# Kernel tuning notes

Hardware: AMD Instinct MI355X
Metric: run time of the kernel (lower is better)

## Reference

```python
import jax, jax.numpy as jnp
import numpy as np

DIM = 2048
RANK = 128


def _xavier_uniform(key, shape, gain=0.5):
    fan_out, fan_in = shape
    limit = gain * np.sqrt(6.0 / (fan_in + fan_out))
    return jax.random.uniform(key, shape, jnp.float32, -limit, limit)


def setup_inputs() -> dict:
    key = jax.random.key(0)
    ks = jax.random.split(key, 6)
    T, B = 1024, 16
    x = jax.random.normal(ks[0], (T, B, DIM), jnp.float32)
    h0 = jax.random.normal(ks[1], (B, DIM), jnp.float32)
    U_x = _xavier_uniform(ks[2], (DIM, RANK))
    V_x = _xavier_uniform(ks[3], (RANK, DIM))
    U_d = _xavier_uniform(ks[4], (DIM, RANK))
    V_d = _xavier_uniform(ks[5], (RANK, DIM))
    r_h = jnp.full((DIM,), 0.9, jnp.float32)
    r_delta = jnp.full((DIM,), 0.1, jnp.float32)
    b = jnp.zeros((DIM,), jnp.float32)
    b_delta = jnp.full((DIM,), -2.0, jnp.float32)
    b_gate = jnp.zeros((DIM,), jnp.float32)
    return {"x": x, "h0": h0, "U_x": U_x, "V_x": V_x, "U_d": U_d, "V_d": V_d,
            "r_h": r_h, "r_delta": r_delta, "b": b, "b_delta": b_delta, "b_gate": b_gate}


def reference(x, h0, U_x, V_x, U_d, V_d, r_h, r_delta, b, b_delta, b_gate):
    # Precompute input projections for all timesteps (batched low-rank GEMMs):
    # W(x) = U @ (V @ x)  ->  [T,B,D]
    wx = jnp.einsum('tbd,rd,or->tbo', x, V_x, U_x)
    wd = jnp.einsum('tbd,rd,or->tbo', x, V_d, U_d)

    def step(h_prev, inp):
        x_t, wx_t, wd_t = inp
        cand = jnp.tanh(r_h * h_prev + wx_t + b)
        delta = jax.nn.sigmoid(wd_t + r_delta * h_prev + b_delta)
        h_new = (1.0 - delta) * h_prev + delta * cand
        g = h_new + x_t + b_gate
        out = h_new * (g * jax.nn.sigmoid(g))  # silu gate
        return h_new, (out, h_new)

    _, (output, hs) = jax.lax.scan(step, h0, (x, wx, wd))
    h = jnp.concatenate([h0[None], hs], axis=0)  # [T+1,B,D]
    return output, h
```

## Files before the change

kernel.cpp:

```cpp
#include <hip/hip_runtime.h>

#define DIMN 2048
#define RANKN 128
#define TT 1024
#define BBATCH 16
#define BD (BBATCH * DIMN)
#define CH 16
#define PADW 68

typedef __attribute__((ext_vector_type(4))) float floatx4;
typedef __attribute__((ext_vector_type(8))) short short8;

__device__ __forceinline__ short f2bf(float f) {
    unsigned u = __float_as_uint(f);
    unsigned r = (u + 0x7FFFu + ((u >> 16) & 1u)) >> 16;
    return (short)r;
}
__device__ __forceinline__ float fast_sigmoid(float z) {
    return 1.0f / (1.0f + __expf(-z));
}
__device__ __forceinline__ float fast_tanh(float z) {
    return 1.0f - 2.0f / (__expf(2.0f * z) + 1.0f);
}

__global__ __launch_bounds__(256)
void prep_vb(const float* __restrict__ Vx, const float* __restrict__ Vd,
             short* __restrict__ Vb) {
    const int gid = blockIdx.x * 256 + threadIdx.x;
    const size_t base = (size_t)gid * 8;
    const size_t half = (size_t)RANKN * DIMN;
    const float* src = (base < half) ? Vx : Vd;
    const size_t off = (base < half) ? base : (base - half);
    float4 a = *(const float4*)(src + off);
    float4 c = *(const float4*)(src + off + 4);
    short8 v;
    v[0] = f2bf(a.x); v[1] = f2bf(a.y); v[2] = f2bf(a.z); v[3] = f2bf(a.w);
    v[4] = f2bf(c.x); v[5] = f2bf(c.y); v[6] = f2bf(c.z); v[7] = f2bf(c.w);
    *(short8*)(Vb + base) = v;
}

__global__ __launch_bounds__(256, 2)
void gemm_xv(const float* __restrict__ X, const short* __restrict__ Vb,
             short* __restrict__ xvb) {
    constexpr int PADK = 40;
    __shared__ short As[32 * PADK];
    __shared__ short Bs[2][128 * PADK];

    const int m0 = blockIdx.x * 32;
    const int tid = threadIdx.x;
    const int wave = tid >> 6;
    const int lane = tid & 63;
    const int lr = lane & 15;
    const int q  = lane >> 4;
    const int mat = wave >> 1;
    const int wn  = (wave & 1) * 64;

    floatx4 acc[2][4] = {};

    for (int k0 = 0; k0 < DIMN; k0 += 32) {
        {
            int r = tid >> 3, c = (tid & 7) * 4;
            float4 v = *(const float4*)(X + (size_t)(m0 + r) * DIMN + k0 + c);
            *(short4*)&As[r * PADK + c] =
                make_short4(f2bf(v.x), f2bf(v.y), f2bf(v.z), f2bf(v.w));
        }
        #pragma unroll
        for (int i = 0; i < 4; ++i) {
            int u = tid + i * 256;
            int bm = u >> 9;
            int rem = u & 511;
            int r = rem >> 2, c8 = (rem & 3) * 8;
            short8 v = *(const short8*)(Vb + ((size_t)bm * RANKN + r) * DIMN + k0 + c8);
            *(short8*)&Bs[bm][r * PADK + c8] = v;
        }
        __syncthreads();

        short8 af[2], bfr[4];
        #pragma unroll
        for (int mi = 0; mi < 2; ++mi)
            af[mi] = *(const short8*)&As[(mi * 16 + lr) * PADK + q * 8];
        #pragma unroll
        for (int nj = 0; nj < 4; ++nj)
            bfr[nj] = *(const short8*)&Bs[mat][(wn + nj * 16 + lr) * PADK + q * 8];

        #pragma unroll
        for (int mi = 0; mi < 2; ++mi)
            #pragma unroll
            for (int nj = 0; nj < 4; ++nj)
                acc[mi][nj] = __builtin_amdgcn_mfma_f32_16x16x32_bf16(
                    af[mi], bfr[nj], acc[mi][nj], 0, 0, 0);
        __syncthreads();
    }

    #pragma unroll
    for (int mi = 0; mi < 2; ++mi)
        #pragma unroll
        for (int nj = 0; nj < 4; ++nj)
            #pragma unroll
            for (int r = 0; r < 4; ++r) {
                int row = m0 + mi * 16 + q * 4 + r;
                int col = mat * RANKN + wn + nj * 16 + lr;
                xvb[(size_t)row * 256 + col] = f2bf(acc[mi][nj][r]);
            }
}

#define SPIN(ctr, tgt) \
    while (((volatile int*)cnt)[ctr] < (tgt)) __builtin_amdgcn_s_sleep(1); \
    asm volatile("" ::: "memory");

#define SIGNAL(ctr, val) \
    asm volatile("" ::: "memory"); \
    if (lane == 0) ((volatile int*)cnt)[ctr] = (val);

#define SIGNAL_AFTER_READS(ctr, val) \
    asm volatile("s_waitcnt lgkmcnt(0)" ::: "memory"); \
    if (lane == 0) ((volatile int*)cnt)[ctr] = (val);

__global__ __launch_bounds__(192, 2)
void fused_scan(const short* __restrict__ xvb, const float* __restrict__ x,
                const float* __restrict__ h0,
                const float* __restrict__ Ux, const float* __restrict__ Ud,
                const float* __restrict__ r_h, const float* __restrict__ r_delta,
                const float* __restrict__ bvec, const float* __restrict__ b_delta,
                const float* __restrict__ b_gate,
                float* __restrict__ obuf, float* __restrict__ hbuf) {
    __shared__ float wxs[2][CH * PADW];
    __shared__ float wds[2][CH * PADW];
    __shared__ float hsh[2][CH * PADW];
    __shared__ short8 Ulds[2][4][4][64];
    __shared__ int cnt[4];

    const int id   = blockIdx.x;
    const int xcd  = id & 7;
    const int slot = id >> 3;
    const int b  = xcd * 2 + (slot & 1);
    const int d0 = (slot >> 1) * 64;

    const int tid  = threadIdx.x;
    const int wave = tid >> 6;
    const int lane = tid & 63;
    const int lr = lane & 15;
    const int q  = lane >> 4;

    if (tid == 0) { cnt[0] = 0; cnt[1] = 0; cnt[2] = 0; cnt[3] = 0; }
    __syncthreads();

    if (wave == 1) {
        #pragma unroll
        for (int mat = 0; mat < 2; ++mat) {
            const float* Up = mat ? Ud : Ux;
            #pragma unroll
            for (int nj = 0; nj < 4; ++nj) {
                const size_t dd = (size_t)(d0 + nj * 16 + lr);
                #pragma unroll
                for (int ks = 0; ks < 4; ++ks) {
                    const int k = ks * 32 + q * 8;
                    float4 u0 = *(const float4*)&Up[dd * RANKN + k];
                    float4 u1 = *(const float4*)&Up[dd * RANKN + k + 4];
                    short8 v;
                    v[0] = f2bf(u0.x); v[1] = f2bf(u0.y);
                    v[2] = f2bf(u0.z); v[3] = f2bf(u0.w);
                    v[4] = f2bf(u1.x); v[5] = f2bf(u1.y);
                    v[6] = f2bf(u1.z); v[7] = f2bf(u1.w);
                    Ulds[mat][nj][ks][lane] = v;
                }
            }
        }
        short8 afp[2][4];
        {
            const size_t row = (size_t)lr * BBATCH + b;
            #pragma unroll
            for (int mat = 0; mat < 2; ++mat)
                #pragma unroll
                for (int ks = 0; ks < 4; ++ks)
                    afp[mat][ks] = *(const short8*)
                        &xvb[row * 256 + mat * RANKN + ks * 32 + q * 8];
        }
        for (int ch = 0; ch < 64; ++ch) {
            if (ch >= 2) { SPIN(1, ch - 1) }
            const int pb = ch & 1;
            #pragma unroll
            for (int mat = 0; mat < 2; ++mat) {
                float* outp = mat ? wds[pb] : wxs[pb];
                #pragma unroll
                for (int nj = 0; nj < 4; ++nj) {
                    floatx4 acc = {};
                    #pragma unroll
                    for (int ks = 0; ks < 4; ++ks)
                        acc = __builtin_amdgcn_mfma_f32_16x16x32_bf16(
                            afp[mat][ks], Ulds[mat][nj][ks][lane], acc, 0, 0, 0);
                    #pragma unroll
                    for (int r = 0; r < 4; ++r)
                        outp[(q * 4 + r) * PADW + nj * 16 + lr] = acc[r];
                }
            }
            SIGNAL(0, ch + 1)
            if (ch < 63) {
                const size_t row = (size_t)((ch + 1) * CH + lr) * BBATCH + b;
                #pragma unroll
                for (int mat = 0; mat < 2; ++mat)
                    #pragma unroll
                    for (int ks = 0; ks < 4; ++ks)
                        afp[mat][ks] = *(const short8*)
                            &xvb[row * 256 + mat * RANKN + ks * 32 + q * 8];
            }
        }
    } else if (wave == 0) {
        const int d = d0 + lane;
        const size_t xo = (size_t)b * DIMN + d;
        const float rh  = r_h[d];
        const float rd  = r_delta[d];
        const float bb  = bvec[d];
        const float bdl = b_delta[d];
        float h = h0[xo];

        for (int ch = 0; ch < 64; ++ch) {
            SPIN(0, ch + 1)
            const int pb = ch & 1;
            float wxr[CH], wdr[CH];
            #pragma unroll
            for (int s = 0; s < CH; ++s) {
                wxr[s] = wxs[pb][s * PADW + lane];
                wdr[s] = wds[pb][s * PADW + lane];
            }
            SIGNAL_AFTER_READS(1, ch + 1)
            if (ch >= 2) { SPIN(3, ch - 1) }
            #pragma unroll
            for (int s = 0; s < CH; ++s) {
                const float cand  = fast_tanh(rh * h + wxr[s] + bb);
                const float delta = fast_sigmoid(wdr[s] + rd * h + bdl);
                h = (1.0f - delta) * h + delta * cand;
                hsh[pb][s * PADW + lane] = h;
            }
            SIGNAL(2, ch + 1)
        }
    } else {
        const int dq  = lane & 15;
        const int tof = lane >> 4;
        const size_t xoffF = (size_t)b * DIMN + d0 + dq * 4;
        const float4 bg4 = *(const float4*)&b_gate[d0 + dq * 4];
        {
            const int dl = d0 + lane;
            (void)dl;
            float4 hv = *(const float4*)&h0[(size_t)b * DIMN + d0 + dq * 4
                                            + (size_t)tof * 0];
            if (tof == 0)
                *(float4*)&hbuf[(size_t)b * DIMN + d0 + dq * 4] = hv;
        }
        float4 xpre[4];
        #pragma unroll
        for (int jj = 0; jj < 4; ++jj)
            xpre[jj] = *(const float4*)&x[(size_t)(jj * 4 + tof) * BD + xoffF];

        for (int ch = 0; ch < 64; ++ch) {
            SPIN(2, ch + 1)
            const int pb = ch & 1;
            float4 hv[4];
            #pragma unroll
            for (int jj = 0; jj < 4; ++jj)
                hv[jj] = *(const float4*)&hsh[pb][(jj * 4 + tof) * PADW + dq * 4];
            SIGNAL_AFTER_READS(3, ch + 1)
            const int tb = ch * CH;
            #pragma unroll
            for (int jj = 0; jj < 4; ++jj) {
                const int t = jj * 4 + tof;
                const float4 xv = xpre[jj];
                float4 ov;
                float g0 = hv[jj].x + xv.x + bg4.x;
                ov.x = hv[jj].x * (g0 * fast_sigmoid(g0));
                float g1 = hv[jj].y + xv.y + bg4.y;
                ov.y = hv[jj].y * (g1 * fast_sigmoid(g1));
                float g2 = hv[jj].z + xv.z + bg4.z;
                ov.z = hv[jj].z * (g2 * fast_sigmoid(g2));
                float g3 = hv[jj].w + xv.w + bg4.w;
                ov.w = hv[jj].w * (g3 * fast_sigmoid(g3));
                *(float4*)&obuf[(size_t)(tb + t) * BD + xoffF] = ov;
                *(float4*)&hbuf[(size_t)(tb + t + 1) * BD + xoffF] = hv[jj];
            }
            if (ch < 63) {
                const int tn = (ch + 1) * CH;
                #pragma unroll
                for (int jj = 0; jj < 4; ++jj)
                    xpre[jj] = *(const float4*)
                        &x[(size_t)(tn + jj * 4 + tof) * BD + xoffF];
            }
        }
    }
}

extern "C" void kernel_launch(void* const* d_in, const int* in_sizes, int n_in,
                              void* d_out, int out_size, void* d_ws, size_t ws_size,
                              hipStream_t stream) {
    const float* x       = (const float*)d_in[0];
    const float* h0      = (const float*)d_in[1];
    const float* U_x     = (const float*)d_in[2];
    const float* V_x     = (const float*)d_in[3];
    const float* U_d     = (const float*)d_in[4];
    const float* V_d     = (const float*)d_in[5];
    const float* r_h     = (const float*)d_in[6];
    const float* r_delta = (const float*)d_in[7];
    const float* bvec    = (const float*)d_in[8];
    const float* b_delta = (const float*)d_in[9];
    const float* b_gate  = (const float*)d_in[10];

    float* obuf = (float*)d_out;
    float* hbuf = obuf + (size_t)TT * BD;
    short* xvb  = (short*)d_ws;
    short* Vb   = xvb + (size_t)TT * BBATCH * 256;

    prep_vb<<<256, 256, 0, stream>>>(V_x, V_d, Vb);

    gemm_xv<<<TT * BBATCH / 32, 256, 0, stream>>>(x, Vb, xvb);

    fused_scan<<<512, 192, 0, stream>>>(xvb, x, h0, U_x, U_d,
                                        r_h, r_delta, bvec, b_delta, b_gate,
                                        obuf, hbuf);
}
```

Measured before the change: 534.8 us.

## Halve per-block dim width, double blocks, deepen LDS ring, keep U in registers

The fused scan now has each block handle 32 hidden dims instead of 64 and launches 1024 blocks, so the serial recurrence is spread over twice as many waves. The chunk ring grows from 2 to 4 slots so the producer and consumer waves can run further ahead. U fragments move from LDS into registers, and wx/wd are interleaved as float2 in one buffer. Sigmoid and tanh use the hardware reciprocal, and launch bounds ask for 3 blocks per CU. The recurrence wave now has half its lanes duplicating work (lane&31), and MFMA efficiency per block drops.

Result: no change. 539.4 us (+0.9%).

```diff
diff --git a/kernel.cpp b/kernel.cpp
--- a/kernel.cpp
+++ b/kernel.cpp
@@ -6,7 +6,9 @@
 #define BBATCH 16
 #define BD (BBATCH * DIMN)
 #define CH 16
-#define PADW 68
+#define NCH (TT / CH)
+#define PITW 66
+#define PITH 36
 
 typedef __attribute__((ext_vector_type(4))) float floatx4;
 typedef __attribute__((ext_vector_type(8))) short short8;
@@ -17,10 +19,10 @@
     return (short)r;
 }
 __device__ __forceinline__ float fast_sigmoid(float z) {
-    return 1.0f / (1.0f + __expf(-z));
+    return __builtin_amdgcn_rcpf(1.0f + __expf(-z));
 }
 __device__ __forceinline__ float fast_tanh(float z) {
-    return 1.0f - 2.0f / (__expf(2.0f * z) + 1.0f);
+    return 1.0f - 2.0f * __builtin_amdgcn_rcpf(__expf(2.0f * z) + 1.0f);
 }
 
 __global__ __launch_bounds__(256)
@@ -116,7 +118,7 @@
     asm volatile("s_waitcnt lgkmcnt(0)" ::: "memory"); \
     if (lane == 0) ((volatile int*)cnt)[ctr] = (val);
 
-__global__ __launch_bounds__(192, 2)
+__global__ __launch_bounds__(192, 3)
 void fused_scan(const short* __restrict__ xvb, const float* __restrict__ x,
                 const float* __restrict__ h0,
                 const float* __restrict__ Ux, const float* __restrict__ Ud,
@@ -124,17 +126,15 @@
                 const float* __restrict__ bvec, const float* __restrict__ b_delta,
                 const float* __restrict__ b_gate,
                 float* __restrict__ obuf, float* __restrict__ hbuf) {
-    __shared__ float wxs[2][CH * PADW];
-    __shared__ float wds[2][CH * PADW];
-    __shared__ float hsh[2][CH * PADW];
-    __shared__ short8 Ulds[2][4][4][64];
+    __shared__ float wwds[4 * CH * PITW];
+    __shared__ float hsd [4 * CH * PITH];
     __shared__ int cnt[4];
 
     const int id   = blockIdx.x;
     const int xcd  = id & 7;
     const int slot = id >> 3;
     const int b  = xcd * 2 + (slot & 1);
-    const int d0 = (slot >> 1) * 64;
+    const int d0 = (slot >> 1) * 32;
 
     const int tid  = threadIdx.x;
     const int wave = tid >> 6;
@@ -146,11 +146,12 @@
     __syncthreads();
 
     if (wave == 1) {
+        short8 uf[2][2][4];
         #pragma unroll
         for (int mat = 0; mat < 2; ++mat) {
             const float* Up = mat ? Ud : Ux;
             #pragma unroll
-            for (int nj = 0; nj < 4; ++nj) {
+            for (int nj = 0; nj < 2; ++nj) {
                 const size_t dd = (size_t)(d0 + nj * 16 + lr);
                 #pragma unroll
                 for (int ks = 0; ks < 4; ++ks) {
@@ -162,7 +163,7 @@
                     v[2] = f2bf(u0.z); v[3] = f2bf(u0.w);
                     v[4] = f2bf(u1.x); v[5] = f2bf(u1.y);
                     v[6] = f2bf(u1.z); v[7] = f2bf(u1.w);
-                    Ulds[mat][nj][ks][lane] = v;
+                    uf[mat][nj][ks] = v;
                 }
             }
         }
@@ -176,26 +177,25 @@
                     afp[mat][ks] = *(const short8*)
                         &xvb[row * 256 + mat * RANKN + ks * 32 + q * 8];
         }
-        for (int ch = 0; ch < 64; ++ch) {
-            if (ch >= 2) { SPIN(1, ch - 1) }
-            const int pb = ch & 1;
-            #pragma unroll
-            for (int mat = 0; mat < 2; ++mat) {
-                float* outp = mat ? wds[pb] : wxs[pb];
-                #pragma unroll
-                for (int nj = 0; nj < 4; ++nj) {
+        for (int ch = 0; ch < NCH; ++ch) {
+            if (ch >= 4) { SPIN(1, ch - 3) }
+            const int sl = ch & 3;
+            #pragma unroll
+            for (int mat = 0; mat < 2; ++mat)
+                #pragma unroll
+                for (int nj = 0; nj < 2; ++nj) {
                     floatx4 acc = {};
                     #pragma unroll
                     for (int ks = 0; ks < 4; ++ks)
                         acc = __builtin_amdgcn_mfma_f32_16x16x32_bf16(
-                            afp[mat][ks], Ulds[mat][nj][ks][lane], acc, 0, 0, 0);
+                            afp[mat][ks], uf[mat][nj][ks], acc, 0, 0, 0);
                     #pragma unroll
                     for (int r = 0; r < 4; ++r)
-                        outp[(q * 4 + r) * PADW + nj * 16 + lr] = acc[r];
+                        wwds[sl * (CH * PITW) + (q * 4 + r) * PITW
+                             + (nj * 16 + lr) * 2 + mat] = acc[r];
                 }
-            }
             SIGNAL(0, ch + 1)
-            if (ch < 63) {
+            if (ch < NCH - 1) {
                 const size_t row = (size_t)((ch + 1) * CH + lr) * BBATCH + b;
                 #pragma unroll
                 for (int mat = 0; mat < 2; ++mat)
@@ -206,7 +206,8 @@
             }
         }
     } else if (wave == 0) {
-        const int d = d0 + lane;
+        const int dcol = lane & 31;
+        const int d = d0 + dcol;
         const size_t xo = (size_t)b * DIMN + d;
         const float rh  = r_h[d];
         const float rd  = r_delta[d];
@@ -214,56 +215,52 @@
         const float bdl = b_delta[d];
         float h = h0[xo];
 
-        for (int ch = 0; ch < 64; ++ch) {
+        for (int ch = 0; ch < NCH; ++ch) {
             SPIN(0, ch + 1)
-            const int pb = ch & 1;
-            float wxr[CH], wdr[CH];
+            const int sl = ch & 3;
+            float2 wv[CH];
+            #pragma unroll
+            for (int s = 0; s < CH; ++s)
+                wv[s] = *(const float2*)
+                    &wwds[sl * (CH * PITW) + s * PITW + dcol * 2];
+            SIGNAL_AFTER_READS(1, ch + 1)
+            if (ch >= 4) { SPIN(3, ch - 3) }
             #pragma unroll
             for (int s = 0; s < CH; ++s) {
-                wxr[s] = wxs[pb][s * PADW + lane];
-                wdr[s] = wds[pb][s * PADW + lane];
-            }
-            SIGNAL_AFTER_READS(1, ch + 1)
-            if (ch >= 2) { SPIN(3, ch - 1) }
-            #pragma unroll
-            for (int s = 0; s < CH; ++s) {
-                const float cand  = fast_tanh(rh * h + wxr[s] + bb);
-                const float delta = fast_sigmoid(wdr[s] + rd * h + bdl);
+                const float cand  = fast_tanh(rh * h + wv[s].x + bb);
+                const float delta = fast_sigmoid(wv[s].y + rd * h + bdl);
                 h = (1.0f - delta) * h + delta * cand;
-                hsh[pb][s * PADW + lane] = h;
+                hsd[sl * (CH * PITH) + s * PITH + dcol] = h;
             }
             SIGNAL(2, ch + 1)
         }
     } else {
-        const int dq  = lane & 15;
-        const int tof = lane >> 4;
+        const int dq  = lane & 7;
+        const int tof = lane >> 3;
         const size_t xoffF = (size_t)b * DIMN + d0 + dq * 4;
         const float4 bg4 = *(const float4*)&b_gate[d0 + dq * 4];
-        {
-            const int dl = d0 + lane;
-            (void)dl;
-            float4 hv = *(const float4*)&h0[(size_t)b * DIMN + d0 + dq * 4
-                                            + (size_t)tof * 0];
-            if (tof == 0)
-                *(float4*)&hbuf[(size_t)b * DIMN + d0 + dq * 4] = hv;
-        }
-        float4 xpre[4];
-        #pragma unroll
-        for (int jj = 0; jj < 4; ++jj)
-            xpre[jj] = *(const float4*)&x[(size_t)(jj * 4 + tof) * BD + xoffF];
-
-        for (int ch = 0; ch < 64; ++ch) {
+        if (tof == 0) {
+            float4 hv = *(const float4*)&h0[xoffF];
+            *(float4*)&hbuf[xoffF] = hv;
+        }
+        float4 xpre[2];
+        #pragma unroll
+        for (int jj = 0; jj < 2; ++jj)
+            xpre[jj] = *(const float4*)&x[(size_t)(jj * 8 + tof) * BD + xoffF];
+
+        for (int ch = 0; ch < NCH; ++ch) {
             SPIN(2, ch + 1)
-            const int pb = ch & 1;
-            float4 hv[4];
-            #pragma unroll
-            for (int jj = 0; jj < 4; ++jj)
-                hv[jj] = *(const float4*)&hsh[pb][(jj * 4 + tof) * PADW + dq * 4];
+            const int sl = ch & 3;
+            float4 hv[2];
+            #pragma unroll
+            for (int jj = 0; jj < 2; ++jj)
+                hv[jj] = *(const float4*)
+                    &hsd[sl * (CH * PITH) + (jj * 8 + tof) * PITH + dq * 4];
             SIGNAL_AFTER_READS(3, ch + 1)
             const int tb = ch * CH;
             #pragma unroll
-            for (int jj = 0; jj < 4; ++jj) {
-                const int t = jj * 4 + tof;
+            for (int jj = 0; jj < 2; ++jj) {
+                const int t = jj * 8 + tof;
                 const float4 xv = xpre[jj];
                 float4 ov;
                 float g0 = hv[jj].x + xv.x + bg4.x;
@@ -277,12 +274,12 @@
                 *(float4*)&obuf[(size_t)(tb + t) * BD + xoffF] = ov;
                 *(float4*)&hbuf[(size_t)(tb + t + 1) * BD + xoffF] = hv[jj];
             }
-            if (ch < 63) {
+            if (ch < NCH - 1) {
                 const int tn = (ch + 1) * CH;
                 #pragma unroll
-                for (int jj = 0; jj < 4; ++jj)
+                for (int jj = 0; jj < 2; ++jj)
                     xpre[jj] = *(const float4*)
-                        &x[(size_t)(tn + jj * 4 + tof) * BD + xoffF];
+                        &x[(size_t)(tn + jj * 8 + tof) * BD + xoffF];
             }
         }
     }
@@ -312,7 +309,7 @@
 
     gemm_xv<<<TT * BBATCH / 32, 256, 0, stream>>>(x, Vb, xvb);
 
-    fused_scan<<<512, 192, 0, stream>>>(xvb, x, h0, U_x, U_d,
-                                        r_h, r_delta, bvec, b_delta, b_gate,
-                                        obuf, hbuf);
-}
+    fused_scan<<<1024, 192, 0, stream>>>(xvb, x, h0, U_x, U_d,
+                                         r_h, r_delta, bvec, b_delta, b_gate,
+                                         obuf, hbuf);
+}
```
